# Kernel optimization log

Hardware: AMD Instinct MI355X
Metric: run time of the kernel (lower is better)

Reference implementation:

```python
import jax, jax.numpy as jnp
import numpy as np

B, G, IN, NC, OUT = 32768, 25, 128, 3, 75
# group id per in_out_map entry: 0=spinal (0-4), 1=nfn (5-14), 2=ss (15-24)
GROUP = jnp.asarray(np.repeat(np.arange(3), [5, 10, 10]).astype(np.int32))


def _linear_init(key, fan_in, shape):
    s = 1.0 / np.sqrt(fan_in)
    return jax.random.uniform(key, shape, minval=-s, maxval=s, dtype=jnp.float32)


def setup_inputs() -> dict:
    key = jax.random.key(0)
    ks = jax.random.split(key, 7)
    x = jax.random.normal(ks[0], (B, G * IN), dtype=jnp.float32)
    # in_out_map: entry i gathers contiguous block i of width IN, scatters to slots 3i..3i+2
    K = jnp.arange(G * IN, dtype=jnp.int32).reshape(G, IN)
    V = jnp.arange(G * NC, dtype=jnp.int32).reshape(G, NC)
    W_spinal = _linear_init(ks[1], IN, (IN, NC))
    b_spinal = _linear_init(ks[2], IN, (NC,))
    W_nfn = _linear_init(ks[3], IN, (IN, NC))
    b_nfn = _linear_init(ks[4], IN, (NC,))
    W_ss = _linear_init(ks[5], IN, (IN, NC))
    b_ss = _linear_init(ks[6], IN, (NC,))
    return dict(x=x, K=K, V=V, W_spinal=W_spinal, b_spinal=b_spinal,
                W_nfn=W_nfn, b_nfn=b_nfn, W_ss=W_ss, b_ss=b_ss)


def reference(x, K, V, W_spinal, b_spinal, W_nfn, b_nfn, W_ss, b_ss):
    # Stack the 3 tiny Linears and broadcast to one weight per map entry: (G, IN, NC)
    W = jnp.stack([W_spinal, W_nfn, W_ss])[GROUP]
    b = jnp.stack([b_spinal, b_nfn, b_ss])[GROUP]        # (G, NC)
    xg = x[:, K]                                         # gather -> (B, G, IN)
    o = jnp.einsum('bgi,gic->bgc', xg, W) + b            # (B, G, NC)
    out = jnp.zeros((x.shape[0], OUT), x.dtype)
    out = out.at[:, V.reshape(-1)].set(o.reshape(x.shape[0], G * 3))  # scatter
    return out
```

## Files before the change

kernel.cpp:

```cpp
#include <hip/hip_runtime.h>


#define NCHUNK    102400
#define GRID_DIM  2048
#define BLOCK_DIM 256

#define FADD_DPP(acc, ctrl, rmask)                                             \
  do {                                                                         \
    int _t = __builtin_amdgcn_update_dpp(0, __float_as_int(acc), (ctrl),       \
                                         (rmask), 0xF, true);                  \
    (acc) += __int_as_float(_t);                                               \
  } while (0)

#define HALF_REDUCE3(a0, a1, a2)                                               \
  do {                                                                         \
    FADD_DPP(a0, 0x111, 0xF); FADD_DPP(a1, 0x111, 0xF); FADD_DPP(a2, 0x111, 0xF); \
    FADD_DPP(a0, 0x112, 0xF); FADD_DPP(a1, 0x112, 0xF); FADD_DPP(a2, 0x112, 0xF); \
    FADD_DPP(a0, 0x114, 0xF); FADD_DPP(a1, 0x114, 0xF); FADD_DPP(a2, 0x114, 0xF); \
    FADD_DPP(a0, 0x118, 0xF); FADD_DPP(a1, 0x118, 0xF); FADD_DPP(a2, 0x118, 0xF); \
    FADD_DPP(a0, 0x142, 0xA); FADD_DPP(a1, 0x142, 0xA); FADD_DPP(a2, 0x142, 0xA); \
  } while (0)

__global__ __launch_bounds__(BLOCK_DIM, 8)
void mlp_rsna9_kernel(const float* __restrict__ x,
                      const float* __restrict__ Wsp, const float* __restrict__ bsp,
                      const float* __restrict__ Wnf, const float* __restrict__ bnf,
                      const float* __restrict__ Wss, const float* __restrict__ bss,
                      float* __restrict__ out)
{
    __shared__ __align__(16) float w_lds[3 * 3 * 128];
    __shared__ float b_lds[12];

    const int tid = threadIdx.x;

    for (int idx = tid; idx < 1152; idx += BLOCK_DIM) {
        int t = idx / 384;
        int r = idx - t * 384;
        int c = r >> 7;
        int i = r & 127;
        const float* wp = (t == 0) ? Wsp : (t == 1) ? Wnf : Wss;
        w_lds[idx] = wp[i * 3 + c];
    }
    if (tid < 9) {
        int t = tid / 3;
        int c = tid - t * 3;
        const float* bp = (t == 0) ? bsp : (t == 1) ? bnf : bss;
        b_lds[tid] = bp[c];
    }
    __syncthreads();

    const int half = tid >> 5;
    const int i0   = (tid & 31) << 2;

    for (int base = blockIdx.x * 2; base < NCHUNK; base += GRID_DIM * 2) {
        const int c0 = base, c1 = base + 1;

        const float4 xv0 = *(const float4*)(x + (size_t)c0 * 1024 + (size_t)tid * 4);
        const float4 xv1 = *(const float4*)(x + (size_t)c1 * 1024 + (size_t)tid * 4);

        const int seg0 = c0 * 8 + half;
        const int seg1 = c1 * 8 + half;
        const int g0 = seg0 % 25;
        const int g1 = seg1 % 25;
        const int t0 = (g0 >= 5) + (g0 >= 15);
        const int t1 = (g1 >= 5) + (g1 >= 15);

        const float* wb0 = w_lds + t0 * 384 + i0;
        const float4 w00 = *(const float4*)(wb0);
        const float4 w01 = *(const float4*)(wb0 + 128);
        const float4 w02 = *(const float4*)(wb0 + 256);
        const float* wb1 = w_lds + t1 * 384 + i0;
        const float4 w10 = *(const float4*)(wb1);
        const float4 w11 = *(const float4*)(wb1 + 128);
        const float4 w12 = *(const float4*)(wb1 + 256);

        float a00 = xv0.x * w00.x + xv0.y * w00.y + xv0.z * w00.z + xv0.w * w00.w;
        float a01 = xv0.x * w01.x + xv0.y * w01.y + xv0.z * w01.z + xv0.w * w01.w;
        float a02 = xv0.x * w02.x + xv0.y * w02.y + xv0.z * w02.z + xv0.w * w02.w;
        float a10 = xv1.x * w10.x + xv1.y * w10.y + xv1.z * w10.z + xv1.w * w10.w;
        float a11 = xv1.x * w11.x + xv1.y * w11.y + xv1.z * w11.z + xv1.w * w11.w;
        float a12 = xv1.x * w12.x + xv1.y * w12.y + xv1.z * w12.z + xv1.w * w12.w;

        HALF_REDUCE3(a00, a01, a02);
        HALF_REDUCE3(a10, a11, a12);

        if ((tid & 31) == 31) {
            float* op0 = out + (size_t)seg0 * 3;
            op0[0] = a00 + b_lds[t0 * 3 + 0];
            op0[1] = a01 + b_lds[t0 * 3 + 1];
            op0[2] = a02 + b_lds[t0 * 3 + 2];
            float* op1 = out + (size_t)seg1 * 3;
            op1[0] = a10 + b_lds[t1 * 3 + 0];
            op1[1] = a11 + b_lds[t1 * 3 + 1];
            op1[2] = a12 + b_lds[t1 * 3 + 2];
        }
    }
}

extern "C" void kernel_launch(void* const* d_in, const int* in_sizes, int n_in,
                              void* d_out, int out_size, void* d_ws, size_t ws_size,
                              hipStream_t stream)
{
    const float* x   = (const float*)d_in[0];
    const float* Wsp = (const float*)d_in[3];
    const float* bsp = (const float*)d_in[4];
    const float* Wnf = (const float*)d_in[5];
    const float* bnf = (const float*)d_in[6];
    const float* Wss = (const float*)d_in[7];
    const float* bss = (const float*)d_in[8];
    float* out = (float*)d_out;

    mlp_rsna9_kernel<<<GRID_DIM, BLOCK_DIM, 0, stream>>>(
        x, Wsp, bsp, Wnf, bnf, Wss, bss, out);
}
```

Before: 560.9 us.

## Give each block a contiguous chunk range and prefetch the next x loads

Each block now processes 50 contiguous 1024-float chunks instead of striding across the grid, loading the next pair of float4s before computing the current pair (software pipelining). Group indices are updated incrementally rather than recomputed with modulo. This is meant to hide global load latency and improve locality of streaming reads and writes, at the cost of extra registers and a redundant final load.

```diff
diff --git a/kernel.cpp b/kernel.cpp
--- a/kernel.cpp
+++ b/kernel.cpp
@@ -1,9 +1,10 @@
 #include <hip/hip_runtime.h>
 
 
-#define NCHUNK    102400
+#define BLOCK_DIM 256
 #define GRID_DIM  2048
-#define BLOCK_DIM 256
+#define CPB       50
+#define ITERS     25
 
 #define FADD_DPP(acc, ctrl, rmask)                                             \
   do {                                                                         \
@@ -52,16 +53,21 @@
     const int half = tid >> 5;
     const int i0   = (tid & 31) << 2;
 
-    for (int base = blockIdx.x * 2; base < NCHUNK; base += GRID_DIM * 2) {
-        const int c0 = base, c1 = base + 1;
+    const int c0 = blockIdx.x * CPB;
+    int g0 = (c0 * 8 + half) % 25;
 
-        const float4 xv0 = *(const float4*)(x + (size_t)c0 * 1024 + (size_t)tid * 4);
-        const float4 xv1 = *(const float4*)(x + (size_t)c1 * 1024 + (size_t)tid * 4);
+    const float* xp = x + (size_t)c0 * 1024 + (size_t)tid * 4;
+    float*       op = out + ((size_t)c0 * 8 + half) * 3;
 
-        const int seg0 = c0 * 8 + half;
-        const int seg1 = c1 * 8 + half;
-        const int g0 = seg0 % 25;
-        const int g1 = seg1 % 25;
+    float4 pA = *(const float4*)(xp);
+    float4 pB = *(const float4*)(xp + 1024);
+
+    for (int j = 0; j < ITERS; ++j) {
+        const float* xn = xp + ((j < ITERS - 1) ? 2048 : 0);
+        float4 nA = *(const float4*)(xn);
+        float4 nB = *(const float4*)(xn + 1024);
+
+        int g1 = g0 + 8; if (g1 >= 25) g1 -= 25;
         const int t0 = (g0 >= 5) + (g0 >= 15);
         const int t1 = (g1 >= 5) + (g1 >= 15);
 
@@ -74,26 +80,29 @@
         const float4 w11 = *(const float4*)(wb1 + 128);
         const float4 w12 = *(const float4*)(wb1 + 256);
 
-        float a00 = xv0.x * w00.x + xv0.y * w00.y + xv0.z * w00.z + xv0.w * w00.w;
-        float a01 = xv0.x * w01.x + xv0.y * w01.y + xv0.z * w01.z + xv0.w * w01.w;
-        float a02 = xv0.x * w02.x + xv0.y * w02.y + xv0.z * w02.z + xv0.w * w02.w;
-        float a10 = xv1.x * w10.x + xv1.y * w10.y + xv1.z * w10.z + xv1.w * w10.w;
-        float a11 = xv1.x * w11.x + xv1.y * w11.y + xv1.z * w11.z + xv1.w * w11.w;
-        float a12 = xv1.x * w12.x + xv1.y * w12.y + xv1.z * w12.z + xv1.w * w12.w;
+        float a00 = pA.x * w00.x + pA.y * w00.y + pA.z * w00.z + pA.w * w00.w;
+        float a01 = pA.x * w01.x + pA.y * w01.y + pA.z * w01.z + pA.w * w01.w;
+        float a02 = pA.x * w02.x + pA.y * w02.y + pA.z * w02.z + pA.w * w02.w;
+        float a10 = pB.x * w10.x + pB.y * w10.y + pB.z * w10.z + pB.w * w10.w;
+        float a11 = pB.x * w11.x + pB.y * w11.y + pB.z * w11.z + pB.w * w11.w;
+        float a12 = pB.x * w12.x + pB.y * w12.y + pB.z * w12.z + pB.w * w12.w;
 
         HALF_REDUCE3(a00, a01, a02);
         HALF_REDUCE3(a10, a11, a12);
 
         if ((tid & 31) == 31) {
-            float* op0 = out + (size_t)seg0 * 3;
-            op0[0] = a00 + b_lds[t0 * 3 + 0];
-            op0[1] = a01 + b_lds[t0 * 3 + 1];
-            op0[2] = a02 + b_lds[t0 * 3 + 2];
-            float* op1 = out + (size_t)seg1 * 3;
-            op1[0] = a10 + b_lds[t1 * 3 + 0];
-            op1[1] = a11 + b_lds[t1 * 3 + 1];
-            op1[2] = a12 + b_lds[t1 * 3 + 2];
+            op[0] = a00 + b_lds[t0 * 3 + 0];
+            op[1] = a01 + b_lds[t0 * 3 + 1];
+            op[2] = a02 + b_lds[t0 * 3 + 2];
+            op[24] = a10 + b_lds[t1 * 3 + 0];
+            op[25] = a11 + b_lds[t1 * 3 + 1];
+            op[26] = a12 + b_lds[t1 * 3 + 2];
         }
+
+        pA = nA; pB = nB;
+        xp += 2048;
+        op += 48;
+        g0 += 16; if (g0 >= 25) g0 -= 25;
     }
 }
 
```

Measured after the change: 567.5 us. Within noise of the previous version (+1.2%).
